# Optimization experiments

Hardware: AMD Instinct MI355X
Metric: run time of the kernel (lower is better)

## Reference

```python
import jax, jax.numpy as jnp
import numpy as np

B, S, D = 4, 4096, 2048
L = 3  # conv kernel size (L_cache)


def setup_inputs() -> dict:
    key = jax.random.key(0)
    k1, k2, k3, k4 = jax.random.split(key, 4)
    scale_in = 1.0 / np.sqrt(D)
    return {
        "x": jax.random.normal(k1, (B, S, D), dtype=jnp.float32),
        "W_in": jax.random.normal(k2, (D, 3 * D), dtype=jnp.float32) * scale_in,
        "conv_w": jax.random.normal(k3, (D, L), dtype=jnp.float32) * (1.0 / np.sqrt(L)),
        "W_out": jax.random.normal(k4, (D, D), dtype=jnp.float32) * scale_in,
    }


def _causal_depthwise_conv(bx, conv_w):
    # bx: [B, D, S], conv_w: [D, L]; causal cross-correlation per channel
    rhs = conv_w[:, None, :]  # [D, 1, L] = (out_ch, in_ch/groups, width)
    return jax.lax.conv_general_dilated(
        bx, rhs,
        window_strides=(1,),
        padding=[(L - 1, 0)],
        dimension_numbers=("NCH", "OIH", "NCH"),
        feature_group_count=bx.shape[1],
    )


def reference(x, W_in, conv_w, W_out):
    # in_proj: [B,S,D] @ [D,3D] -> [B,S,3D]
    BCx = jnp.einsum("bsd,de->bse", x, W_in)
    B_gate, C_gate, x_proj = jnp.split(BCx, 3, axis=-1)  # each [B,S,D]
    Bx = (B_gate * x_proj).transpose(0, 2, 1)            # [B,D,S]
    conv_out = _causal_depthwise_conv(Bx, conv_w)         # [B,D,S]
    y = C_gate * conv_out.transpose(0, 2, 1)              # [B,S,D]
    return jnp.einsum("bsd,de->bse", y, W_out)            # [B,S,D]
```

## Files before the change

kernel.cpp:

```cpp
#include <hip/hip_runtime.h>
#include <cstddef>
#include <cstdint>

#define D_DIM 2048
#define S_DIM 4096
#define B_DIM 4
#define M_DIM (B_DIM * S_DIM)
#define N1_DIM (3 * D_DIM)

typedef short bf16x8 __attribute__((ext_vector_type(8)));
typedef float f32x4  __attribute__((ext_vector_type(4)));

typedef const unsigned int __attribute__((address_space(1))) gu32_t;
typedef unsigned int       __attribute__((address_space(3))) lu32_t;

__device__ __forceinline__ unsigned short f2bf(float f) {
    unsigned int u = __float_as_uint(f);
    u += 0x7FFFu + ((u >> 16) & 1u);
    return (unsigned short)(u >> 16);
}
__device__ __forceinline__ float bf2f(unsigned short h) {
    return __uint_as_float(((unsigned int)h) << 16);
}

__global__ void k_convert(const float* __restrict__ in, unsigned short* __restrict__ out, int n8) {
    int i = blockIdx.x * blockDim.x + threadIdx.x;
    if (i >= n8) return;
    const float4* p = (const float4*)in + (size_t)i * 2;
    float4 a = p[0];
    float4 b = p[1];
    union { unsigned short s[8]; uint4 v; } r;
    r.s[0] = f2bf(a.x); r.s[1] = f2bf(a.y); r.s[2] = f2bf(a.z); r.s[3] = f2bf(a.w);
    r.s[4] = f2bf(b.x); r.s[5] = f2bf(b.y); r.s[6] = f2bf(b.z); r.s[7] = f2bf(b.w);
    ((uint4*)out)[i] = r.v;
}

__global__ void k_transpose(const float* __restrict__ in, unsigned short* __restrict__ out,
                            int R, int C) {
    __shared__ float t[32][33];
    int c0 = blockIdx.x * 32, r0 = blockIdx.y * 32;
    int x = threadIdx.x;
    for (int yy = threadIdx.y; yy < 32; yy += 8)
        t[yy][x] = in[(size_t)(r0 + yy) * C + c0 + x];
    __syncthreads();
    for (int yy = threadIdx.y; yy < 32; yy += 8)
        out[(size_t)(c0 + yy) * R + r0 + x] = f2bf(t[x][yy]);
}

template <bool OUT_BF16>
__global__ __launch_bounds__(256, 2)
void k_gemm(const unsigned short* __restrict__ A, const unsigned short* __restrict__ Bt,
            void* __restrict__ Cp, int N, int K) {
    __shared__ unsigned short As[128 * 64];
    __shared__ unsigned short Bs[128 * 64];

    const int tid  = threadIdx.x;
    const int wave = tid >> 6;
    const int lane = tid & 63;
    const int m0 = blockIdx.y * 128;
    const int n0 = blockIdx.x * 128;
    const int wm = (wave & 1) * 64;
    const int wn = (wave >> 1) * 64;

    f32x4 acc[4][4] = {};

    const int srow = lane >> 3;
    const int gd   = lane & 7;
    const int quad = lane >> 4;
    const int rsel = lane & 15;

    const int KT = K >> 6;
    for (int kt = 0; kt < KT; ++kt) {
        const int k0 = kt << 6;
        __syncthreads();
        #pragma unroll
        for (int i = 0; i < 4; ++i) {
            const int seg = i * 4 + wave;
            const int row = seg * 8 + srow;
            const int gs  = gd ^ (row & 7);
            const unsigned short* ga = A  + (size_t)(m0 + row) * K + k0 + gs * 8;
            const unsigned short* gb = Bt + (size_t)(n0 + row) * K + k0 + gs * 8;
            __builtin_amdgcn_global_load_lds((gu32_t*)ga, (lu32_t*)(As + seg * 512), 16, 0, 0);
            __builtin_amdgcn_global_load_lds((gu32_t*)gb, (lu32_t*)(Bs + seg * 512), 16, 0, 0);
        }
        __syncthreads();

        #pragma unroll
        for (int kb = 0; kb < 2; ++kb) {
            bf16x8 af[4], bfr[4];
            #pragma unroll
            for (int i = 0; i < 4; ++i) {
                const int ra = wm + i * 16 + rsel;
                const int ga = (kb * 4 + quad) ^ (ra & 7);
                af[i] = *(const bf16x8*)&As[ra * 64 + ga * 8];
                const int rb = wn + i * 16 + rsel;
                const int gb = (kb * 4 + quad) ^ (rb & 7);
                bfr[i] = *(const bf16x8*)&Bs[rb * 64 + gb * 8];
            }
            #pragma unroll
            for (int i = 0; i < 4; ++i)
                #pragma unroll
                for (int j = 0; j < 4; ++j)
                    acc[i][j] = __builtin_amdgcn_mfma_f32_16x16x32_bf16(af[i], bfr[j], acc[i][j], 0, 0, 0);
        }
    }

    #pragma unroll
    for (int i = 0; i < 4; ++i) {
        #pragma unroll
        for (int j = 0; j < 4; ++j) {
            const int col  = n0 + wn + j * 16 + rsel;
            const int rowb = m0 + wm + i * 16 + quad * 4;
            #pragma unroll
            for (int r = 0; r < 4; ++r) {
                const size_t off = (size_t)(rowb + r) * N + col;
                if (OUT_BF16) ((unsigned short*)Cp)[off] = f2bf(acc[i][j][r]);
                else          ((float*)Cp)[off] = acc[i][j][r];
            }
        }
    }
}

__global__ void k_conv_gate(const unsigned short* __restrict__ BCx,
                            const float* __restrict__ conv_w,
                            unsigned short* __restrict__ y) {
    const int bs = blockIdx.x;
    const int s  = bs & (S_DIM - 1);
    const int d0 = threadIdx.x * 8;
    const size_t row = (size_t)bs * N1_DIM;

    union U8 { uint4 v; unsigned short s[8]; };
    float bx_m2[8], bx_m1[8], bx_0[8];
    #pragma unroll
    for (int j = 0; j < 8; ++j) { bx_m2[j] = 0.f; bx_m1[j] = 0.f; }

    U8 g, xp;
    g.v  = *(const uint4*)&BCx[row + d0];
    xp.v = *(const uint4*)&BCx[row + 2 * D_DIM + d0];
    #pragma unroll
    for (int j = 0; j < 8; ++j) bx_0[j] = bf2f(g.s[j]) * bf2f(xp.s[j]);

    if (s >= 1) {
        g.v  = *(const uint4*)&BCx[row - N1_DIM + d0];
        xp.v = *(const uint4*)&BCx[row - N1_DIM + 2 * D_DIM + d0];
        #pragma unroll
        for (int j = 0; j < 8; ++j) bx_m1[j] = bf2f(g.s[j]) * bf2f(xp.s[j]);
    }
    if (s >= 2) {
        g.v  = *(const uint4*)&BCx[row - 2 * N1_DIM + d0];
        xp.v = *(const uint4*)&BCx[row - 2 * N1_DIM + 2 * D_DIM + d0];
        #pragma unroll
        for (int j = 0; j < 8; ++j) bx_m2[j] = bf2f(g.s[j]) * bf2f(xp.s[j]);
    }

    U8 c; c.v = *(const uint4*)&BCx[row + D_DIM + d0];
    U8 r;
    #pragma unroll
    for (int j = 0; j < 8; ++j) {
        const float* w = conv_w + (size_t)(d0 + j) * 3;
        const float conv = w[0] * bx_m2[j] + w[1] * bx_m1[j] + w[2] * bx_0[j];
        r.s[j] = f2bf(bf2f(c.s[j]) * conv);
    }
    *(uint4*)&y[(size_t)bs * D_DIM + d0] = r.v;
}

extern "C" void kernel_launch(void* const* d_in, const int* in_sizes, int n_in,
                              void* d_out, int out_size, void* d_ws, size_t ws_size,
                              hipStream_t stream) {
    const float* x      = (const float*)d_in[0];
    const float* W_in   = (const float*)d_in[1];
    const float* conv_w = (const float*)d_in[2];
    const float* W_out  = (const float*)d_in[3];
    float* out = (float*)d_out;

    char* ws = (char*)d_ws;
    unsigned short* xb     = (unsigned short*)ws;
    unsigned short* Wt_in  = (unsigned short*)(ws + (size_t)67108864);
    unsigned short* Wt_out = (unsigned short*)(ws + (size_t)67108864 + 25165824);
    unsigned short* BCx    = (unsigned short*)(ws + (size_t)67108864 + 25165824 + 8388608);

    const int n8 = M_DIM * D_DIM / 8;
    k_convert<<<dim3((n8 + 255) / 256), 256, 0, stream>>>(x, xb, n8);
    k_transpose<<<dim3(N1_DIM / 32, D_DIM / 32), dim3(32, 8), 0, stream>>>(W_in, Wt_in, D_DIM, N1_DIM);
    k_transpose<<<dim3(D_DIM / 32, D_DIM / 32), dim3(32, 8), 0, stream>>>(W_out, Wt_out, D_DIM, D_DIM);

    k_gemm<true><<<dim3(N1_DIM / 128, M_DIM / 128), 256, 0, stream>>>(xb, Wt_in, BCx, N1_DIM, D_DIM);
    k_conv_gate<<<dim3(M_DIM), 256, 0, stream>>>(BCx, conv_w, xb );
    k_gemm<false><<<dim3(D_DIM / 128, M_DIM / 128), 256, 0, stream>>>(xb, Wt_out, out, D_DIM, D_DIM);
}
```

Measured before the change: 856.7 us.

## Fuse causal conv and gating into the in-projection GEMM epilogue

```diff
diff --git a/kernel.cpp b/kernel.cpp
--- a/kernel.cpp
+++ b/kernel.cpp
@@ -47,10 +47,139 @@
         out[(size_t)(c0 + yy) * R + r0 + x] = f2bf(t[x][yy]);
 }
 
-template <bool OUT_BF16>
+__global__ void k_transpose_wp(const float* __restrict__ in, unsigned short* __restrict__ out) {
+    __shared__ float t[32][33];
+    int c0 = blockIdx.x * 32, r0 = blockIdx.y * 32;
+    int x = threadIdx.x;
+    for (int yy = threadIdx.y; yy < 32; yy += 8)
+        t[yy][x] = in[(size_t)(r0 + yy) * N1_DIM + c0 + x];
+    __syncthreads();
+    for (int yy = threadIdx.y; yy < 32; yy += 8) {
+        const int n = c0 + yy;
+        const int p = n >> 11, d = n & 2047;
+        const int orow = (d >> 6) * 192 + p * 64 + (d & 63);
+        out[(size_t)orow * D_DIM + r0 + x] = f2bf(t[x][yy]);
+    }
+}
+
 __global__ __launch_bounds__(256, 2)
-void k_gemm(const unsigned short* __restrict__ A, const unsigned short* __restrict__ Bt,
-            void* __restrict__ Cp, int N, int K) {
+void k_gemm_fused(const unsigned short* __restrict__ A, const unsigned short* __restrict__ Wp,
+                  const float* __restrict__ conv_w, unsigned short* __restrict__ Y) {
+    __shared__ __align__(16) char smem[59392];
+    unsigned short* As = (unsigned short*)smem;
+    unsigned short* Bs = (unsigned short*)(smem + 18432);
+    float* BxL         = (float*)smem;
+    unsigned short* yL = (unsigned short*)(smem + 43008);
+
+    const int tid  = threadIdx.x;
+    const int wave = tid >> 6;
+    const int lane = tid & 63;
+    const int m0  = blockIdx.y * 128;
+    const int d0g = blockIdx.x * 64;
+    const int wp0 = blockIdx.x * 192;
+
+    const int srow = lane >> 3;
+    const int gd   = lane & 7;
+    const int quad = lane >> 4;
+    const int rsel = lane & 15;
+
+    f32x4 acc[2][12] = {};
+    f32x4 accH1 = {}, accH2 = {};
+
+    const int K = D_DIM;
+    const int KT = K >> 6;
+    for (int kt = 0; kt < KT; ++kt) {
+        const int k0 = kt << 6;
+        __syncthreads();
+        #pragma unroll
+        for (int i = 0; i < 5; ++i) {
+            const int seg = i * 4 + wave;
+            if (seg < 18) {
+                int rowg = m0 - 16 + seg * 8 + srow;
+                if (rowg < 0) rowg = 0;
+                const int gs = gd ^ srow;
+                const unsigned short* ga = A + (size_t)rowg * K + k0 + gs * 8;
+                __builtin_amdgcn_global_load_lds((gu32_t*)ga, (lu32_t*)(As + seg * 512), 16, 0, 0);
+            }
+        }
+        #pragma unroll
+        for (int i = 0; i < 6; ++i) {
+            const int seg = i * 4 + wave;
+            const int gs = gd ^ srow;
+            const unsigned short* gb = Wp + (size_t)(wp0 + seg * 8 + srow) * K + k0 + gs * 8;
+            __builtin_amdgcn_global_load_lds((gu32_t*)gb, (lu32_t*)(Bs + seg * 512), 16, 0, 0);
+        }
+        __syncthreads();
+
+        #pragma unroll
+        for (int kb = 0; kb < 2; ++kb) {
+            const int gsw = ((kb * 4 + quad) ^ (rsel & 7)) * 8;
+            bf16x8 af[2], bfr[12];
+            const bf16x8 afh = *(const bf16x8*)&As[rsel * 64 + gsw];
+            #pragma unroll
+            for (int i = 0; i < 2; ++i)
+                af[i] = *(const bf16x8*)&As[(16 + wave * 32 + i * 16 + rsel) * 64 + gsw];
+            #pragma unroll
+            for (int j = 0; j < 12; ++j)
+                bfr[j] = *(const bf16x8*)&Bs[(j * 16 + rsel) * 64 + gsw];
+            #pragma unroll
+            for (int i = 0; i < 2; ++i)
+                #pragma unroll
+                for (int j = 0; j < 12; ++j)
+                    acc[i][j] = __builtin_amdgcn_mfma_f32_16x16x32_bf16(af[i], bfr[j], acc[i][j], 0, 0, 0);
+            accH1 = __builtin_amdgcn_mfma_f32_16x16x32_bf16(afh, bfr[wave],     accH1, 0, 0, 0);
+            accH2 = __builtin_amdgcn_mfma_f32_16x16x32_bf16(afh, bfr[8 + wave], accH2, 0, 0, 0);
+        }
+    }
+
+    __syncthreads();
+    #pragma unroll
+    for (int i = 0; i < 2; ++i)
+        #pragma unroll
+        for (int jd = 0; jd < 4; ++jd)
+            #pragma unroll
+            for (int r = 0; r < 4; ++r) {
+                const int row = wave * 32 + i * 16 + quad * 4 + r;
+                const int d   = jd * 16 + rsel;
+                BxL[(row + 2) * 65 + d] = acc[i][jd][r] * acc[i][8 + jd][r];
+            }
+    const bool szero = ((m0 & (S_DIM - 1)) == 0);
+    if (quad == 3) {
+        #pragma unroll
+        for (int r = 2; r < 4; ++r) {
+            const int d = wave * 16 + rsel;
+            BxL[(r - 2) * 65 + d] = szero ? 0.f : (accH1[r] * accH2[r]);
+        }
+    }
+    __syncthreads();
+    #pragma unroll
+    for (int jd = 0; jd < 4; ++jd) {
+        const int d = jd * 16 + rsel;
+        const float* w = conv_w + (size_t)(d0g + d) * 3;
+        const float w0 = w[0], w1 = w[1], w2 = w[2];
+        #pragma unroll
+        for (int i = 0; i < 2; ++i)
+            #pragma unroll
+            for (int r = 0; r < 4; ++r) {
+                const int row = wave * 32 + i * 16 + quad * 4 + r;
+                const float conv = w0 * BxL[row * 65 + d]
+                                 + w1 * BxL[(row + 1) * 65 + d]
+                                 + w2 * BxL[(row + 2) * 65 + d];
+                yL[row * 64 + d] = f2bf(acc[i][4 + jd][r] * conv);
+            }
+    }
+    __syncthreads();
+    #pragma unroll
+    for (int k = 0; k < 4; ++k) {
+        const int u = k * 256 + tid;
+        const int row = u >> 3, cg = u & 7;
+        *(uint4*)&Y[(size_t)(m0 + row) * D_DIM + d0g + cg * 8] = *(const uint4*)&yL[row * 64 + cg * 8];
+    }
+}
+
+__global__ __launch_bounds__(256, 2)
+void k_gemm2(const unsigned short* __restrict__ A, const unsigned short* __restrict__ Bt,
+             float* __restrict__ Cp, int N, int K) {
     __shared__ unsigned short As[128 * 64];
     __shared__ unsigned short Bs[128 * 64];
 
@@ -106,62 +235,15 @@
     }
 
     #pragma unroll
-    for (int i = 0; i < 4; ++i) {
+    for (int i = 0; i < 4; ++i)
         #pragma unroll
         for (int j = 0; j < 4; ++j) {
             const int col  = n0 + wn + j * 16 + rsel;
             const int rowb = m0 + wm + i * 16 + quad * 4;
             #pragma unroll
-            for (int r = 0; r < 4; ++r) {
-                const size_t off = (size_t)(rowb + r) * N + col;
-                if (OUT_BF16) ((unsigned short*)Cp)[off] = f2bf(acc[i][j][r]);
-                else          ((float*)Cp)[off] = acc[i][j][r];
-            }
-        }
-    }
-}
-
-__global__ void k_conv_gate(const unsigned short* __restrict__ BCx,
-                            const float* __restrict__ conv_w,
-                            unsigned short* __restrict__ y) {
-    const int bs = blockIdx.x;
-    const int s  = bs & (S_DIM - 1);
-    const int d0 = threadIdx.x * 8;
-    const size_t row = (size_t)bs * N1_DIM;
-
-    union U8 { uint4 v; unsigned short s[8]; };
-    float bx_m2[8], bx_m1[8], bx_0[8];
-    #pragma unroll
-    for (int j = 0; j < 8; ++j) { bx_m2[j] = 0.f; bx_m1[j] = 0.f; }
-
-    U8 g, xp;
-    g.v  = *(const uint4*)&BCx[row + d0];
-    xp.v = *(const uint4*)&BCx[row + 2 * D_DIM + d0];
-    #pragma unroll
-    for (int j = 0; j < 8; ++j) bx_0[j] = bf2f(g.s[j]) * bf2f(xp.s[j]);
-
-    if (s >= 1) {
-        g.v  = *(const uint4*)&BCx[row - N1_DIM + d0];
-        xp.v = *(const uint4*)&BCx[row - N1_DIM + 2 * D_DIM + d0];
-        #pragma unroll
-        for (int j = 0; j < 8; ++j) bx_m1[j] = bf2f(g.s[j]) * bf2f(xp.s[j]);
-    }
-    if (s >= 2) {
-        g.v  = *(const uint4*)&BCx[row - 2 * N1_DIM + d0];
-        xp.v = *(const uint4*)&BCx[row - 2 * N1_DIM + 2 * D_DIM + d0];
-        #pragma unroll
-        for (int j = 0; j < 8; ++j) bx_m2[j] = bf2f(g.s[j]) * bf2f(xp.s[j]);
-    }
-
-    U8 c; c.v = *(const uint4*)&BCx[row + D_DIM + d0];
-    U8 r;
-    #pragma unroll
-    for (int j = 0; j < 8; ++j) {
-        const float* w = conv_w + (size_t)(d0 + j) * 3;
-        const float conv = w[0] * bx_m2[j] + w[1] * bx_m1[j] + w[2] * bx_0[j];
-        r.s[j] = f2bf(bf2f(c.s[j]) * conv);
-    }
-    *(uint4*)&y[(size_t)bs * D_DIM + d0] = r.v;
+            for (int r = 0; r < 4; ++r)
+                Cp[(size_t)(rowb + r) * N + col] = acc[i][j][r];
+        }
 }
 
 extern "C" void kernel_launch(void* const* d_in, const int* in_sizes, int n_in,
@@ -175,16 +257,15 @@
 
     char* ws = (char*)d_ws;
     unsigned short* xb     = (unsigned short*)ws;
-    unsigned short* Wt_in  = (unsigned short*)(ws + (size_t)67108864);
+    unsigned short* Wp     = (unsigned short*)(ws + (size_t)67108864);
     unsigned short* Wt_out = (unsigned short*)(ws + (size_t)67108864 + 25165824);
-    unsigned short* BCx    = (unsigned short*)(ws + (size_t)67108864 + 25165824 + 8388608);
+    unsigned short* y      = (unsigned short*)(ws + (size_t)67108864 + 25165824 + 8388608);
 
     const int n8 = M_DIM * D_DIM / 8;
     k_convert<<<dim3((n8 + 255) / 256), 256, 0, stream>>>(x, xb, n8);
-    k_transpose<<<dim3(N1_DIM / 32, D_DIM / 32), dim3(32, 8), 0, stream>>>(W_in, Wt_in, D_DIM, N1_DIM);
+    k_transpose_wp<<<dim3(N1_DIM / 32, D_DIM / 32), dim3(32, 8), 0, stream>>>(W_in, Wp);
     k_transpose<<<dim3(D_DIM / 32, D_DIM / 32), dim3(32, 8), 0, stream>>>(W_out, Wt_out, D_DIM, D_DIM);
 
-    k_gemm<true><<<dim3(N1_DIM / 128, M_DIM / 128), 256, 0, stream>>>(xb, Wt_in, BCx, N1_DIM, D_DIM);
-    k_conv_gate<<<dim3(M_DIM), 256, 0, stream>>>(BCx, conv_w, xb );
-    k_gemm<false><<<dim3(D_DIM / 128, M_DIM / 128), 256, 0, stream>>>(xb, Wt_out, out, D_DIM, D_DIM);
-}
+    k_gemm_fused<<<dim3(D_DIM / 64, M_DIM / 128), 256, 0, stream>>>(xb, Wp, conv_w, y);
+    k_gemm2<<<dim3(D_DIM / 128, M_DIM / 128), 256, 0, stream>>>(y, Wt_out, out, D_DIM, D_DIM);
+}
```

After: 2.593 ms. 203% more time.
